# Performance work log

Hardware: AMD Instinct MI355X
Metric: run time of the kernel (lower is better)

## Reference

```python
import math
import jax, jax.numpy as jnp
from jax import lax
import numpy as np

SQRT2 = 1.4142135623730951
LR_MLP = 0.01


def _blur_kernel():
    k = jnp.array([1., 3., 3., 1.], dtype=jnp.float32)
    k = k[:, None] * k[None, :]
    return k / jnp.sum(k)


def upfirdn2d(x, kernel, up, pad0, pad1):
    # x: (B,C,H,W). Matches torch upfirdn2d_native (flip kernel, zero-upsample, pad, correlate).
    B, C, H, W = x.shape
    x = x.reshape(B * C, 1, H, W)
    k = jnp.flip(kernel, (0, 1))[None, None]
    p1 = pad1 + (up - 1)  # lax lhs_dilation omits trailing zeros of upfirdn upsampling
    out = lax.conv_general_dilated(x, k, (1, 1), ((pad0, p1), (pad0, p1)), lhs_dilation=(up, up))
    return out.reshape(B, C, out.shape[-2], out.shape[-1])


def pixel_norm(x, eps=1e-6):
    norm = jnp.sqrt(jnp.sum(x * x, axis=1, keepdims=True))
    norm = norm / math.sqrt(x.shape[1])
    return x / (norm + eps)


def fused_act(x, b):
    return jax.nn.leaky_relu(x + b[None, :, None, None], 0.2) * SQRT2


def mod_conv(x, w, sw, sb, lat, demodulate, up):
    # w: (Cout,Cin,kh,kw); sw: (Cin, style_ch) equalized-lr linear; lat: (B, style_ch)
    Cout, Cin, kh, kw = w.shape
    s = lat @ (sw.T * (1.0 / math.sqrt(sw.shape[1]))) + sb  # (B, Cin), bias_init=1
    wm = (w * (1.0 / math.sqrt(Cin * kh * kw)))[None] * s[:, None, :, None, None]
    if demodulate:
        d = lax.rsqrt(jnp.sum(wm * wm, axis=(2, 3, 4)) + 1e-8)
        wm = wm * d[:, :, None, None, None]
    if up:
        # per-sample conv_transpose(stride=2, pad=0) == dilated conv with flipped kernel
        def f(xi, wi):
            return lax.conv_general_dilated(xi[None], jnp.flip(wi, (2, 3)), (1, 1),
                                            ((kh - 1, kh - 1), (kw - 1, kw - 1)),
                                            lhs_dilation=(2, 2))[0]
        out = jax.vmap(f)(x, wm)
        out = upfirdn2d(out, _blur_kernel() * 4.0, 1, 1, 1)  # Blur pad=(1,1), k*factor^2
    else:
        pad = kh // 2
        def f(xi, wi):
            return lax.conv_general_dilated(xi[None], wi, (1, 1), ((pad, pad), (pad, pad)))[0]
        out = jax.vmap(f)(x, wm)
    return out


def style_mapping(z, W, Bv):
    x = pixel_norm(z)
    sc = 1.0 / math.sqrt(W.shape[-1])
    for i in range(W.shape[0]):
        x = jax.nn.leaky_relu(x @ (W[i].T * sc) + Bv[i] * LR_MLP, 0.2) * SQRT2
    return x


def setup_inputs() -> dict:
    key = jax.random.key(0)
    ks = jax.random.split(key, 32)
    B = 32
    inp = {
        'z': jax.random.normal(ks[0], (B, 512), jnp.float32),
        'mlp_w': jax.random.normal(ks[1], (8, 512, 512), jnp.float32),
        'mlp_b': jax.random.normal(ks[2], (8, 512), jnp.float32),
        'const_input': jax.random.normal(ks[3], (1, 512, 4, 4), jnp.float32),
        'conv_w': jax.random.normal(ks[4], (9, 512, 512, 3, 3), jnp.float32),
        'conv_style_w': jax.random.normal(ks[5], (9, 512, 512), jnp.float32),
        'conv_style_b': jnp.ones((9, 512), jnp.float32),
        'noise_w': jax.random.normal(ks[6], (9,), jnp.float32),
        'act_bias': jnp.zeros((9, 512), jnp.float32),
        'torgb_w': jax.random.normal(ks[7], (5, 3, 512, 1, 1), jnp.float32),
        'torgb_style_w': jax.random.normal(ks[8], (5, 512, 512), jnp.float32),
        'torgb_style_b': jnp.ones((5, 512), jnp.float32),
        'torgb_bias': jnp.zeros((5, 3), jnp.float32),
    }
    sizes = [4, 8, 8, 16, 16, 32, 32, 64, 64]
    for i, s in enumerate(sizes):
        inp[f'noise{i}'] = jax.random.normal(ks[10 + i], (B, 1, s, s), jnp.float32)
    return inp


def reference(z, mlp_w, mlp_b, const_input, conv_w, conv_style_w, conv_style_b,
              noise_w, act_bias, torgb_w, torgb_style_w, torgb_style_b, torgb_bias,
              noise0, noise1, noise2, noise3, noise4, noise5, noise6, noise7, noise8):
    noises = [noise0, noise1, noise2, noise3, noise4, noise5, noise6, noise7, noise8]
    w = style_mapping(z, mlp_w, mlp_b)  # single style injection -> same w for all layers
    B = z.shape[0]
    x = jnp.tile(const_input, (B, 1, 1, 1))

    def sconv(x, i, up):
        out = mod_conv(x, conv_w[i], conv_style_w[i], conv_style_b[i], w, True, up)
        out = out + noise_w[i] * noises[i]
        return fused_act(out, act_bias[i])

    def trgb(x, j):
        out = mod_conv(x, torgb_w[j], torgb_style_w[j], torgb_style_b[j], w, False, False)
        return out + torgb_bias[j][None, :, None, None]

    x = sconv(x, 0, False)
    skip = trgb(x, 0)
    bk = _blur_kernel() * 4.0
    for r in range(4):  # resolutions 8,16,32,64
        x = sconv(x, 1 + 2 * r, True)
        x = sconv(x, 2 + 2 * r, False)
        skip = trgb(x, r + 1) + upfirdn2d(skip, bk, 2, 2, 1)  # UpsampleUpFIRDn pad=(2,1)
    return skip  # (B,3,64,64)
```

## Files before the change

### kernel.cpp

```cpp
#include <hip/hip_runtime.h>
#include <hip/hip_bf16.h>
#include <cstdio>
#include <math.h>


static constexpr int NB = 32;
static constexpr float SQRT2F      = 1.41421356237309515f;
static constexpr float INV_SQRT512 = 0.04419417382415922f;
static constexpr float INV_SQRT4608= 0.014731391274719742f;

typedef __hip_bfloat16 bf16;
typedef __attribute__((ext_vector_type(8))) short bf16x8;
typedef __attribute__((ext_vector_type(4))) float f32x4;

__device__ __forceinline__ float lrelu_s2(float v){ return (v > 0.f ? v : 0.2f*v) * SQRT2F; }
__device__ __forceinline__ float bf_lo(unsigned u){ unsigned v = u << 16; return __builtin_bit_cast(float, v); }
__device__ __forceinline__ float bf_hi(unsigned u){ unsigned v = u & 0xffff0000u; return __builtin_bit_cast(float, v); }
__device__ __forceinline__ unsigned packbf2(float a, float b){
  bf16 ha = __float2bfloat16(a), hb = __float2bfloat16(b);
  unsigned short ra = __builtin_bit_cast(unsigned short, ha);
  unsigned short rb = __builtin_bit_cast(unsigned short, hb);
  return (unsigned)ra | ((unsigned)rb << 16);
}

__global__ void k_mapping(const float* __restrict__ z, const float* __restrict__ mlp_w,
                          const float* __restrict__ mlp_b, float* __restrict__ wlat){
  __shared__ float xb[512], yb[512], red[256];
  int b = blockIdx.x, t = threadIdx.x;
  float z0 = z[b*512 + t], z1 = z[b*512 + t + 256];
  red[t] = z0*z0 + z1*z1;
  __syncthreads();
  for(int s = 128; s > 0; s >>= 1){ if(t < s) red[t] += red[t+s]; __syncthreads(); }
  float norm = sqrtf(red[0]) * INV_SQRT512;
  float inv = 1.f / (norm + 1e-6f);
  xb[t] = z0*inv; xb[t+256] = z1*inv;
  __syncthreads();
  for(int l = 0; l < 8; l++){
    const float* Wl = mlp_w + (size_t)l*512*512;
    const float* bl = mlp_b + l*512;
    for(int oo = 0; oo < 2; oo++){
      int o = t + oo*256;
      const float4* wr = (const float4*)(Wl + (size_t)o*512);
      float acc = 0.f;
      #pragma unroll 4
      for(int k = 0; k < 128; k++){
        float4 w4 = wr[k];
        acc += w4.x*xb[4*k] + w4.y*xb[4*k+1] + w4.z*xb[4*k+2] + w4.w*xb[4*k+3];
      }
      yb[o] = lrelu_s2(acc*INV_SQRT512 + bl[o]*0.01f);
    }
    __syncthreads();
    xb[t] = yb[t]; xb[t+256] = yb[t+256];
    __syncthreads();
  }
  wlat[b*512+t] = xb[t]; wlat[b*512+t+256] = xb[t+256];
}

__global__ void k_styles(const float* __restrict__ wlat,
                         const float* __restrict__ csw, const float* __restrict__ csb,
                         const float* __restrict__ tsw, const float* __restrict__ tsb,
                         float* __restrict__ s_conv, float* __restrict__ s_trgb){
  int gid = blockIdx.x*256 + threadIdx.x;
  int l = gid >> 14;
  int b = (gid >> 9) & 31;
  int i = gid & 511;
  const float* row; float bias, wsc;
  if(l < 9){ row = csw + ((size_t)l*512 + i)*512; bias = csb[l*512+i]; wsc = INV_SQRT4608; }
  else     { int lt = l-9; row = tsw + ((size_t)lt*512 + i)*512; bias = tsb[lt*512+i]; wsc = INV_SQRT512; }
  const float4* r4 = (const float4*)row;
  const float4* w4 = (const float4*)(wlat + b*512);
  float acc = 0.f;
  #pragma unroll 4
  for(int k = 0; k < 128; k++){
    float4 a = w4[k], c = r4[k];
    acc += a.x*c.x + a.y*c.y + a.z*c.z + a.w*c.w;
  }
  float s = (acc*INV_SQRT512 + bias) * wsc;
  if(l < 9) s_conv[((size_t)l*32 + b)*512 + i] = s;
  else      s_trgb[((size_t)(l-9)*32 + b)*512 + i] = s;
}

__global__ void k_prep(const float* __restrict__ cw, float* __restrict__ wsq,
                       bf16* __restrict__ wB){
  int gid = blockIdx.x*256 + threadIdx.x;
  const float* p = cw + (size_t)gid*9;
  int l = gid >> 18;
  int oi = gid & 0x3ffff;
  float v[9]; float a = 0.f;
  #pragma unroll
  for(int t = 0; t < 9; t++){ v[t] = p[t]; a += v[t]*v[t]; }
  wsq[gid] = a;
  #pragma unroll
  for(int tap = 0; tap < 9; tap++)
    wB[((size_t)(l*9 + tap) << 18) + oi] = __float2bfloat16(v[tap]);
}

__global__ void k_demod(const float* __restrict__ s_conv, const float* __restrict__ wsq,
                        float* __restrict__ d_conv){
  __shared__ float s2[512];
  int l = blockIdx.x/32, b = blockIdx.x%32, t = threadIdx.x;
  size_t base = ((size_t)l*32 + b)*512;
  float v0 = s_conv[base + t], v1 = s_conv[base + t + 256];
  s2[t] = v0*v0; s2[t+256] = v1*v1;
  __syncthreads();
  for(int oo = 0; oo < 2; oo++){
    int o = t + oo*256;
    const float4* wr = (const float4*)(wsq + ((size_t)l*512 + o)*512);
    float acc = 0.f;
    #pragma unroll 4
    for(int k = 0; k < 128; k++){
      float4 w = wr[k];
      acc += w.x*s2[4*k] + w.y*s2[4*k+1] + w.z*s2[4*k+2] + w.w*s2[4*k+3];
    }
    d_conv[base + o] = rsqrtf(acc + 1e-8f);
  }
}

__global__ void k_ratio(const float* __restrict__ s_conv, const float* __restrict__ s_trgb,
                        float* __restrict__ rat){
  int gid = blockIdx.x*256 + threadIdx.x;
  int lt = gid >> 14;
  if(lt >= 4){ rat[gid] = 1.0f; return; }
  int b = (gid >> 9) & 31;
  int i = gid & 511;
  int cl = 1 + 2*lt;
  float st = s_trgb[((size_t)lt*32 + b)*512 + i];
  float sc = s_conv[((size_t)cl*32 + b)*512 + i];
  rat[gid] = (sc != 0.f) ? st/sc : 0.f;
}

__global__ void k_init(const float* __restrict__ ci, const float* __restrict__ s_conv,
                       bf16* __restrict__ act){
  int gid = blockIdx.x*256 + threadIdx.x;
  int c = gid & 511; int px = (gid >> 9) & 15; int b = gid >> 13;
  act[gid] = __float2bfloat16(ci[c*16 + px] * s_conv[b*512 + c]);
}

template<bool UP>
__global__ __launch_bounds__(256, 2)
void k_conv(const bf16* __restrict__ act, const bf16* __restrict__ wL,
            const float* __restrict__ dL, const float* __restrict__ noise,
            const float* __restrict__ nw_ptr, const float* __restrict__ ab,
            const float* __restrict__ sN, bf16* __restrict__ outp,
            int Hin, int Mblocks){
  const int q8 = gridDim.x >> 3;
  const int swz = (blockIdx.x & 7)*q8 + (blockIdx.x >> 3);
  const int nb = swz & 3, mb = swz >> 2;
  if(mb >= Mblocks) return;
  const int mbase = mb*128, nbase = nb*128;

  int py = 0, px = 0;
  int OHy, OHx;
  if(UP){
    int cls = blockIdx.z; py = cls >> 1; px = cls & 1;
    OHy = Hin + 1 - py; OHx = Hin + 1 - px;
  } else {
    OHy = Hin; OHx = Hin;
  }
  const int pixN = OHy*OHx;
  const int Mtot = NB*pixN;
  if(mbase >= Mtot) return;

  __shared__ short As[128*64];
  __shared__ short Bs[128*64];
  const int t = threadIdx.x;
  const int row  = t >> 1;
  const int half = t & 1;
  const int r7   = row & 7;

  int m = mbase + row;
  const bool mval = (m < Mtot);
  int mm = mval ? m : 0;
  const int gb = mm / pixN; int rem = mm % pixN;
  const int gY = rem / OHx, gX = rem % OHx;

  const int wid = t >> 6;
  const int mrow0 = (wid >> 1)*64;
  const int ncol0 = (wid & 1)*64;
  const int lr = t & 15;
  const int ks = (t & 63) >> 4;
  const int lr7 = lr & 7;
  const int sw0 = (ks ^ lr7)*8;
  const int sw1 = ((4 + ks) ^ lr7)*8;

  int wsl[4];
  #pragma unroll
  for(int j = 0; j < 4; j++) wsl[j] = ((half*4 + j) ^ r7)*8;

  f32x4 acc[4][4];
  #pragma unroll
  for(int i = 0; i < 4; i++)
    #pragma unroll
    for(int j = 0; j < 4; j++) acc[i][j] = (f32x4){0.f,0.f,0.f,0.f};

  int dyl[3], dxl[3], ndy, ndx;
  if(UP){
    if(py == 0){ dyl[0]=0; dyl[1]=2; ndy=2; } else { dyl[0]=1; ndy=1; }
    if(px == 0){ dxl[0]=0; dxl[1]=2; ndx=2; } else { dxl[0]=1; ndx=1; }
  } else {
    dyl[0]=0; dyl[1]=1; dyl[2]=2; ndy=3;
    dxl[0]=0; dxl[1]=1; dxl[2]=2; ndx=3;
  }
  const int TT = ndy*ndx;

  const bf16* browB = wL + ((size_t)(nbase + row) << 9) + half*32;

  for(int tt = 0; tt < TT; tt++){
    const int dy = dyl[tt/ndx], dx = dxl[tt%ndx];
    const int tap = dy*3 + dx;
    bool aok = false; const bf16* aptr = act;
    {
      int yy, xx;
      if(UP){ yy = gY - ((dy - py) >> 1); xx = gX - ((dx - px) >> 1); }
      else  { yy = gY + dy - 1;           xx = gX + dx - 1; }
      if(mval && (unsigned)yy < (unsigned)Hin && (unsigned)xx < (unsigned)Hin){
        aok = true;
        aptr = act + ((size_t)((gb*Hin + yy)*Hin + xx) << 9) + half*32;
      }
    }
    const bf16* bptr = browB + ((size_t)tap << 18);

    uint4 pa[4], pb[4];
    #pragma unroll
    for(int j = 0; j < 4; j++){
      pa[j] = aok ? *(const uint4*)(aptr + j*8) : make_uint4(0u,0u,0u,0u);
      pb[j] = *(const uint4*)(bptr + j*8);
    }

    #pragma unroll
    for(int c = 0; c < 8; c++){
      asm volatile("" ::: "memory");
      __builtin_amdgcn_s_barrier();
      #pragma unroll
      for(int j = 0; j < 4; j++){
        *(uint4*)&As[row*64 + wsl[j]] = pa[j];
        *(uint4*)&Bs[row*64 + wsl[j]] = pb[j];
      }
      uint4 na[4], nb4[4];
      if(c < 7){
        const int koff = (c+1)*64;
        #pragma unroll
        for(int j = 0; j < 4; j++){
          na[j]  = aok ? *(const uint4*)(aptr + koff + j*8) : make_uint4(0u,0u,0u,0u);
          nb4[j] = *(const uint4*)(bptr + koff + j*8);
        }
      }
      asm volatile("s_waitcnt lgkmcnt(0)" ::: "memory");
      __builtin_amdgcn_s_barrier();
      #pragma unroll
      for(int h = 0; h < 2; h++){
        const int swr = h ? sw1 : sw0;
        bf16x8 af[4], bfr[4];
        #pragma unroll
        for(int f = 0; f < 4; f++){
          af[f]  = *(const bf16x8*)&As[(mrow0 + f*16 + lr)*64 + swr];
          bfr[f] = *(const bf16x8*)&Bs[(ncol0 + f*16 + lr)*64 + swr];
        }
        #pragma unroll
        for(int mf = 0; mf < 4; mf++)
          #pragma unroll
          for(int nf = 0; nf < 4; nf++)
            acc[mf][nf] = __builtin_amdgcn_mfma_f32_16x16x32_bf16(af[mf], bfr[nf], acc[mf][nf], 0, 0, 0);
      }
      if(c < 7){
        #pragma unroll
        for(int j = 0; j < 4; j++){ pa[j] = na[j]; pb[j] = nb4[j]; }
      }
    }
  }

  const float nwv = UP ? 0.f : *nw_ptr;
  const int U = 2*Hin + 1;
  #pragma unroll
  for(int mf = 0; mf < 4; mf++){
    #pragma unroll
    for(int r = 0; r < 4; r++){
      int me = mbase + mrow0 + mf*16 + ks*4 + r;
      if(me >= Mtot) continue;
      int b = me / pixN; int rem2 = me % pixN; int y = rem2 / OHx, x = rem2 % OHx;
      const float* drow = dL + b*512;
      bf16* orow;
      float nz = 0.f; const float* srow = nullptr;
      if(UP){
        orow = outp + (((size_t)((b*U + 2*y + py))*U + (2*x + px)) << 9);
      } else {
        nz = nwv * noise[(b*OHy + y)*OHx + x];
        srow = sN + b*512;
        orow = outp + ((size_t)me << 9);
      }
      #pragma unroll
      for(int nf = 0; nf < 4; nf++){
        int n = nbase + ncol0 + nf*16 + lr;
        float val = acc[mf][nf][r] * drow[n];
        if(!UP) val = lrelu_s2(val + nz + ab[n]) * srow[n];
        orow[n] = __float2bfloat16(val);
      }
    }
  }
}

__global__ void k_blurV(const bf16* __restrict__ u, bf16* __restrict__ tmp, int O){
  const int U = O + 1;
  size_t gid = (size_t)blockIdx.x*256 + threadIdx.x;
  size_t total = (size_t)NB*O*U*128;
  if(gid >= total) return;
  int c4 = gid & 127;
  size_t pix = gid >> 7;
  int X = pix % U; int Y = (pix/U) % O; int b = pix/((size_t)O*U);
  const float k1[4] = {0.25f, 0.75f, 0.75f, 0.25f};
  float4 a = make_float4(0.f,0.f,0.f,0.f);
  #pragma unroll
  for(int ky = 0; ky < 4; ky++){
    int yy = Y + ky - 1; if(yy < 0 || yy >= U) continue;
    float w = k1[ky];
    uint2 u2 = *(const uint2*)(u + (((size_t)(b*U + yy)*U + X) << 9) + c4*4);
    a.x += w*bf_lo(u2.x); a.y += w*bf_hi(u2.x);
    a.z += w*bf_lo(u2.y); a.w += w*bf_hi(u2.y);
  }
  uint2 pk;
  pk.x = packbf2(a.x, a.y); pk.y = packbf2(a.z, a.w);
  *(uint2*)(tmp + (pix << 9) + c4*4) = pk;
}

__global__ void k_blurH(const bf16* __restrict__ tmp, const float* __restrict__ noise,
                        const float* __restrict__ nw_ptr, const float* __restrict__ ab,
                        const float* __restrict__ sN, bf16* __restrict__ act, int O){
  const int U = O + 1;
  size_t gid = (size_t)blockIdx.x*256 + threadIdx.x;
  size_t total = (size_t)NB*O*O*128;
  if(gid >= total) return;
  int c4 = gid & 127;
  size_t pix = gid >> 7;
  int X = pix % O; int Y = (pix/O) % O; int b = pix/((size_t)O*O);
  const float k1[4] = {0.25f, 0.75f, 0.75f, 0.25f};
  float4 a = make_float4(0.f,0.f,0.f,0.f);
  #pragma unroll
  for(int kx = 0; kx < 4; kx++){
    int xx = X + kx - 1; if(xx < 0 || xx >= U) continue;
    float w = k1[kx];
    uint2 u2 = *(const uint2*)(tmp + (((size_t)(b*O + Y)*U + xx) << 9) + c4*4);
    a.x += w*bf_lo(u2.x); a.y += w*bf_hi(u2.x);
    a.z += w*bf_lo(u2.y); a.w += w*bf_hi(u2.y);
  }
  float nz = (*nw_ptr) * noise[(b*O + Y)*O + X];
  const float* abp4 = ab + c4*4;
  float4 s4 = *(const float4*)(sN + b*512 + c4*4);
  uint2 pk;
  pk.x = packbf2(lrelu_s2(a.x + nz + abp4[0])*s4.x, lrelu_s2(a.y + nz + abp4[1])*s4.y);
  pk.y = packbf2(lrelu_s2(a.z + nz + abp4[2])*s4.z, lrelu_s2(a.w + nz + abp4[3])*s4.w);
  *(uint2*)(act + (pix << 9) + c4*4) = pk;
}

__global__ void k_torgb(const bf16* __restrict__ act, const float* __restrict__ tw,
                        const float* __restrict__ ratL, const float* __restrict__ tbias,
                        float* __restrict__ dst, int H, int lt, int addflag){
  int wid = threadIdx.x >> 6, lane = threadIdx.x & 63;
  int pix = blockIdx.x*4 + wid;
  int npix = NB*H*H;
  if(pix >= npix) return;
  int b = pix/(H*H);
  const bf16* ap = act + ((size_t)pix << 9);
  const float* rp = ratL + (size_t)b*512;
  const float* w0 = tw + ((size_t)lt*3 + 0)*512;
  const float* w1 = tw + ((size_t)lt*3 + 1)*512;
  const float* w2 = tw + ((size_t)lt*3 + 2)*512;
  float a0 = 0.f, a1 = 0.f, a2 = 0.f;
  #pragma unroll
  for(int j = 0; j < 8; j++){
    int i = lane + j*64;
    float xs = __bfloat162float(ap[i])*rp[i];
    a0 += xs*w0[i]; a1 += xs*w1[i]; a2 += xs*w2[i];
  }
  for(int off = 32; off > 0; off >>= 1){
    a0 += __shfl_xor(a0, off);
    a1 += __shfl_xor(a1, off);
    a2 += __shfl_xor(a2, off);
  }
  if(lane == 0){
    int rem = pix % (H*H);
    size_t o0 = ((size_t)(b*3 + 0)*H*H) + rem;
    size_t o1 = ((size_t)(b*3 + 1)*H*H) + rem;
    size_t o2 = ((size_t)(b*3 + 2)*H*H) + rem;
    float b0 = tbias[lt*3+0], b1 = tbias[lt*3+1], b2 = tbias[lt*3+2];
    if(addflag){ dst[o0] += a0 + b0; dst[o1] += a1 + b1; dst[o2] += a2 + b2; }
    else       { dst[o0]  = a0 + b0; dst[o1]  = a1 + b1; dst[o2]  = a2 + b2; }
  }
}

__global__ void k_skipup(const float* __restrict__ sin, float* __restrict__ sout, int h){
  const int O = 2*h;
  int gid = blockIdx.x*256 + threadIdx.x;
  int total = NB*3*O*O;
  if(gid >= total) return;
  int X = gid % O; int Y = (gid/O) % O; int c = (gid/(O*O)) % 3; int b = gid/(3*O*O);
  const float k1[4] = {1.f, 3.f, 3.f, 1.f};
  float acc = 0.f;
  for(int ky = (Y & 1); ky < 4; ky += 2){
    int ty = Y + ky - 2;
    if(ty < 0) continue;
    int y = ty >> 1; if(y >= h) continue;
    for(int kx = (X & 1); kx < 4; kx += 2){
      int tx = X + kx - 2;
      if(tx < 0) continue;
      int x = tx >> 1; if(x >= h) continue;
      acc += k1[ky]*k1[kx]*(1.f/16.f) * sin[((size_t)(b*3 + c)*h + y)*h + x];
    }
  }
  sout[gid] = acc;
}

extern "C" void kernel_launch(void* const* d_in, const int* in_sizes, int n_in,
                              void* d_out, int out_size, void* d_ws, size_t ws_size,
                              hipStream_t stream){
  const float* z     = (const float*)d_in[0];
  const float* mlp_w = (const float*)d_in[1];
  const float* mlp_b = (const float*)d_in[2];
  const float* cinp  = (const float*)d_in[3];
  const float* conv_w= (const float*)d_in[4];
  const float* csw   = (const float*)d_in[5];
  const float* csb   = (const float*)d_in[6];
  const float* nwp   = (const float*)d_in[7];
  const float* abp   = (const float*)d_in[8];
  const float* tw    = (const float*)d_in[9];
  const float* tsw   = (const float*)d_in[10];
  const float* tsb   = (const float*)d_in[11];
  const float* tb    = (const float*)d_in[12];
  const float* noise[9];
  for(int i = 0; i < 9; i++) noise[i] = (const float*)d_in[13 + i];

  const size_t UMAX = (size_t)32*65*65*512;
  char* base = (char*)d_ws;
  size_t off = 0;
  bf16* buf0 = (bf16*)(base + off); off += UMAX*2;
  bf16* buf1 = (bf16*)(base + off); off += UMAX*2;
  bf16* wB   = (bf16*)(base + off); off += (size_t)9*9*512*512*2;
  float* wsq = (float*)(base + off); off += (size_t)9*512*512*4;
  float* wlat= (float*)(base + off); off += (size_t)32*512*4;
  float* sconv=(float*)(base + off); off += (size_t)9*32*512*4;
  float* dconv=(float*)(base + off); off += (size_t)9*32*512*4;
  float* strgb=(float*)(base + off); off += (size_t)5*32*512*4;
  float* rat  =(float*)(base + off); off += (size_t)5*32*512*4;
  float* skipA=(float*)(base + off); off += (size_t)32*3*64*64*4;
  float* skipB=(float*)(base + off); off += (size_t)32*3*64*64*4;
  if(ws_size < off){
    fprintf(stderr, "kernel_launch: ws too small (%zu < %zu)\n", ws_size, off);
    return;
  }
  float* out = (float*)d_out;

  k_mapping<<<32, 256, 0, stream>>>(z, mlp_w, mlp_b, wlat);
  k_styles <<<896, 256, 0, stream>>>(wlat, csw, csb, tsw, tsb, sconv, strgb);
  k_prep   <<<9216, 256, 0, stream>>>(conv_w, wsq, wB);
  k_demod  <<<288, 256, 0, stream>>>(sconv, wsq, dconv);
  k_ratio  <<<320, 256, 0, stream>>>(sconv, strgb, rat);
  k_init   <<<1024, 256, 0, stream>>>(cinp, sconv, buf0);

  auto conv_noup = [&](const bf16* in, bf16* o, int H, int layer, const float* sN){
    int M = 32*H*H; int Mb = (M + 127)/128;
    int Gx = ((Mb*4 + 7)/8)*8;
    k_conv<false><<<dim3(Gx,1,1), 256, 0, stream>>>(in, wB + ((size_t)layer*9 << 18),
        dconv + (size_t)layer*NB*512, noise[layer], nwp + layer, abp + layer*512, sN, o, H, Mb);
  };
  auto conv_up = [&](const bf16* in, bf16* o, int Hin, int layer){
    int Mmax = 32*(Hin+1)*(Hin+1); int Mb = (Mmax + 127)/128;
    int Gx = ((Mb*4 + 7)/8)*8;
    k_conv<true><<<dim3(Gx,1,4), 256, 0, stream>>>(in, wB + ((size_t)layer*9 << 18),
        dconv + (size_t)layer*NB*512, nullptr, nullptr, nullptr, nullptr, o, Hin, Mb);
  };
  auto blur = [&](const bf16* u, bf16* tmp, bf16* o, int O, int layer, const float* sN){
    size_t totV = (size_t)32*O*(O+1)*128;
    size_t totH = (size_t)32*O*O*128;
    k_blurV<<<(unsigned)((totV + 255)/256), 256, 0, stream>>>(u, tmp, O);
    k_blurH<<<(unsigned)((totH + 255)/256), 256, 0, stream>>>(tmp, noise[layer], nwp + layer,
        abp + layer*512, sN, o, O);
  };
  auto torgb = [&](const bf16* act, float* dst, int H, int lt, int add){
    int npix = 32*H*H;
    k_torgb<<<(npix + 3)/4, 256, 0, stream>>>(act, tw, rat + (size_t)lt*NB*512, tb, dst, H, lt, add);
  };
  auto skipup = [&](const float* sin, float* sout, int h){
    int total = 32*3*(2*h)*(2*h);
    k_skipup<<<(total + 255)/256, 256, 0, stream>>>(sin, sout, h);
  };

  const float* S = sconv;
  const float* sT4 = strgb + (size_t)4*NB*512;

  conv_noup(buf0, buf1, 4, 0, S + (size_t)1*NB*512);
  torgb(buf1, skipA, 4, 0, 0);

  conv_up(buf1, buf0, 4, 1);
  blur(buf0, buf1, buf0, 8, 1, S + (size_t)2*NB*512);
  conv_noup(buf0, buf1, 8, 2, S + (size_t)3*NB*512);
  skipup(skipA, skipB, 4);
  torgb(buf1, skipB, 8, 1, 1);

  conv_up(buf1, buf0, 8, 3);
  blur(buf0, buf1, buf0, 16, 3, S + (size_t)4*NB*512);
  conv_noup(buf0, buf1, 16, 4, S + (size_t)5*NB*512);
  skipup(skipB, skipA, 8);
  torgb(buf1, skipA, 16, 2, 1);

  conv_up(buf1, buf0, 16, 5);
  blur(buf0, buf1, buf0, 32, 5, S + (size_t)6*NB*512);
  conv_noup(buf0, buf1, 32, 6, S + (size_t)7*NB*512);
  skipup(skipA, skipB, 16);
  torgb(buf1, skipB, 32, 3, 1);

  conv_up(buf1, buf0, 32, 7);
  blur(buf0, buf1, buf0, 64, 7, S + (size_t)8*NB*512);
  conv_noup(buf0, buf1, 64, 8, sT4);
  skipup(skipB, out, 32);
  torgb(buf1, out, 64, 4, 1);
}
```

Before: 2.204 ms.

## Add 256x256-tile implicit-GEMM conv kernel for large non-upsampling layers

Adds k_conv2, a 512-thread implicit-GEMM 3x3 conv kernel with 256x256 output tiles and register-prefetched global loads double-staged into swizzled LDS. It is used for non-upsampling layers at 32x32 and 64x64, and the original 128-tile kernel is kept for smaller resolutions. The larger tiles are meant to raise arithmetic intensity and cut repeated weight and activation loads. In exchange each thread holds 32 accumulator vectors (high register pressure at launch bounds 512,2), uses 64KB of shared memory per block, and launches fewer blocks.

```diff
diff --git a/kernel.cpp b/kernel.cpp
--- a/kernel.cpp
+++ b/kernel.cpp
@@ -299,6 +299,141 @@
   }
 }
 
+__global__ __launch_bounds__(512, 2)
+void k_conv2(const bf16* __restrict__ act, const bf16* __restrict__ wL,
+             const float* __restrict__ dL, const float* __restrict__ noise,
+             const float* __restrict__ nw_ptr, const float* __restrict__ ab,
+             const float* __restrict__ sN, bf16* __restrict__ outp,
+             int Hin, int Mblocks){
+  const int q8 = gridDim.x >> 3;
+  const int swz = (blockIdx.x & 7)*q8 + (blockIdx.x >> 3);
+  const int nb = swz & 1, mb = swz >> 1;
+  if(mb >= Mblocks) return;
+  const int mbase = mb*256, nbase = nb*256;
+  const int pixN = Hin*Hin;
+  const int Mtot = NB*pixN;
+  if(mbase >= Mtot) return;
+
+  __shared__ short As[256*64];
+  __shared__ short Bs[256*64];
+  const int t = threadIdx.x;
+  const int row  = t >> 1;
+  const int half = t & 1;
+  const int r7   = row & 7;
+
+  int m = mbase + row;
+  const bool mval = (m < Mtot);
+  int mm = mval ? m : 0;
+  const int gb = mm / pixN; int rem = mm % pixN;
+  const int gY = rem / Hin, gX = rem % Hin;
+
+  const int wid = t >> 6;
+  const int mrow0 = (wid >> 2)*128;
+  const int ncol0 = (wid & 3)*64;
+  const int lr = t & 15;
+  const int ks = (t & 63) >> 4;
+  const int lr7 = lr & 7;
+  const int sw0 = (ks ^ lr7)*8;
+  const int sw1 = ((4 + ks) ^ lr7)*8;
+
+  int wsl[4];
+  #pragma unroll
+  for(int j = 0; j < 4; j++) wsl[j] = ((half*4 + j) ^ r7)*8;
+
+  f32x4 acc[8][4];
+  #pragma unroll
+  for(int i = 0; i < 8; i++)
+    #pragma unroll
+    for(int j = 0; j < 4; j++) acc[i][j] = (f32x4){0.f,0.f,0.f,0.f};
+
+  const bf16* browB = wL + ((size_t)(nbase + row) << 9) + half*32;
+
+  for(int tt = 0; tt < 9; tt++){
+    const int dy = tt/3, dx = tt - dy*3;
+    const int tap = tt;
+    bool aok = false; const bf16* aptr = act;
+    {
+      int yy = gY + dy - 1, xx = gX + dx - 1;
+      if(mval && (unsigned)yy < (unsigned)Hin && (unsigned)xx < (unsigned)Hin){
+        aok = true;
+        aptr = act + ((size_t)((gb*Hin + yy)*Hin + xx) << 9) + half*32;
+      }
+    }
+    const bf16* bptr = browB + ((size_t)tap << 18);
+
+    uint4 pa[4], pb[4];
+    #pragma unroll
+    for(int j = 0; j < 4; j++){
+      pa[j] = aok ? *(const uint4*)(aptr + j*8) : make_uint4(0u,0u,0u,0u);
+      pb[j] = *(const uint4*)(bptr + j*8);
+    }
+
+    #pragma unroll
+    for(int c = 0; c < 8; c++){
+      asm volatile("" ::: "memory");
+      __builtin_amdgcn_s_barrier();
+      #pragma unroll
+      for(int j = 0; j < 4; j++){
+        *(uint4*)&As[row*64 + wsl[j]] = pa[j];
+        *(uint4*)&Bs[row*64 + wsl[j]] = pb[j];
+      }
+      uint4 na[4], nb4[4];
+      if(c < 7){
+        const int koff = (c+1)*64;
+        #pragma unroll
+        for(int j = 0; j < 4; j++){
+          na[j]  = aok ? *(const uint4*)(aptr + koff + j*8) : make_uint4(0u,0u,0u,0u);
+          nb4[j] = *(const uint4*)(bptr + koff + j*8);
+        }
+      }
+      asm volatile("s_waitcnt lgkmcnt(0)" ::: "memory");
+      __builtin_amdgcn_s_barrier();
+      #pragma unroll
+      for(int h = 0; h < 2; h++){
+        const int swr = h ? sw1 : sw0;
+        bf16x8 af[8], bfr[4];
+        #pragma unroll
+        for(int f = 0; f < 8; f++)
+          af[f]  = *(const bf16x8*)&As[(mrow0 + f*16 + lr)*64 + swr];
+        #pragma unroll
+        for(int f = 0; f < 4; f++)
+          bfr[f] = *(const bf16x8*)&Bs[(ncol0 + f*16 + lr)*64 + swr];
+        #pragma unroll
+        for(int mf = 0; mf < 8; mf++)
+          #pragma unroll
+          for(int nf = 0; nf < 4; nf++)
+            acc[mf][nf] = __builtin_amdgcn_mfma_f32_16x16x32_bf16(af[mf], bfr[nf], acc[mf][nf], 0, 0, 0);
+      }
+      if(c < 7){
+        #pragma unroll
+        for(int j = 0; j < 4; j++){ pa[j] = na[j]; pb[j] = nb4[j]; }
+      }
+    }
+  }
+
+  const float nwv = *nw_ptr;
+  #pragma unroll
+  for(int mf = 0; mf < 8; mf++){
+    #pragma unroll
+    for(int r = 0; r < 4; r++){
+      int me = mbase + mrow0 + mf*16 + ks*4 + r;
+      if(me >= Mtot) continue;
+      int b = me / pixN; int rem2 = me % pixN; int y = rem2 / Hin, x = rem2 % Hin;
+      const float* drow = dL + b*512;
+      float nz = nwv * noise[(b*Hin + y)*Hin + x];
+      const float* srow = sN + b*512;
+      bf16* orow = outp + ((size_t)me << 9);
+      #pragma unroll
+      for(int nf = 0; nf < 4; nf++){
+        int n = nbase + ncol0 + nf*16 + lr;
+        float val = acc[mf][nf][r] * drow[n];
+        val = lrelu_s2(val + nz + ab[n]) * srow[n];
+        orow[n] = __float2bfloat16(val);
+      }
+    }
+  }
+}
+
 __global__ void k_blurV(const bf16* __restrict__ u, bf16* __restrict__ tmp, int O){
   const int U = O + 1;
   size_t gid = (size_t)blockIdx.x*256 + threadIdx.x;
@@ -456,10 +591,17 @@
   k_init   <<<1024, 256, 0, stream>>>(cinp, sconv, buf0);
 
   auto conv_noup = [&](const bf16* in, bf16* o, int H, int layer, const float* sN){
-    int M = 32*H*H; int Mb = (M + 127)/128;
-    int Gx = ((Mb*4 + 7)/8)*8;
-    k_conv<false><<<dim3(Gx,1,1), 256, 0, stream>>>(in, wB + ((size_t)layer*9 << 18),
-        dconv + (size_t)layer*NB*512, noise[layer], nwp + layer, abp + layer*512, sN, o, H, Mb);
+    if(H >= 32){
+      int M = 32*H*H; int Mb = (M + 255)/256;
+      int Gx = ((Mb*2 + 7)/8)*8;
+      k_conv2<<<dim3(Gx,1,1), 512, 0, stream>>>(in, wB + ((size_t)layer*9 << 18),
+          dconv + (size_t)layer*NB*512, noise[layer], nwp + layer, abp + layer*512, sN, o, H, Mb);
+    } else {
+      int M = 32*H*H; int Mb = (M + 127)/128;
+      int Gx = ((Mb*4 + 7)/8)*8;
+      k_conv<false><<<dim3(Gx,1,1), 256, 0, stream>>>(in, wB + ((size_t)layer*9 << 18),
+          dconv + (size_t)layer*NB*512, noise[layer], nwp + layer, abp + layer*512, sN, o, H, Mb);
+    }
   };
   auto conv_up = [&](const bf16* in, bf16* o, int Hin, int layer){
     int Mmax = 32*(Hin+1)*(Hin+1); int Mb = (Mmax + 127)/128;
```

Measured after the change: 2.165 ms. Within noise of the previous version (-1.7%).

## Double-buffer conv GEMM tiles via direct global-to-LDS loads across taps

Applied to the files above, without the earlier changes.

Replaces the register-staged global→LDS copy in the implicit-GEMM conv with global_load_lds direct loads into double-buffered shared tiles. The next K-chunk, or the first chunk of the next tap, is prefetched while MFMAs run on the current buffer. Out-of-bounds rows point at a zeroed scratch page instead of using predicated zeros. This is meant to hide global load latency and cut VGPR pressure. It doubles LDS use to 64KB per block, which may limit occupancy with launch_bounds(256,2), and it depends on correct vmcnt accounting.

```diff
diff --git a/kernel.cpp b/kernel.cpp
--- a/kernel.cpp
+++ b/kernel.cpp
@@ -12,6 +12,10 @@
 typedef __hip_bfloat16 bf16;
 typedef __attribute__((ext_vector_type(8))) short bf16x8;
 typedef __attribute__((ext_vector_type(4))) float f32x4;
+
+#define GLOAD_LDS16(src, dst) __builtin_amdgcn_global_load_lds( \
+    (const __attribute__((address_space(1))) void*)(src), \
+    (__attribute__((address_space(3))) void*)(dst), 16, 0, 0)
 
 __device__ __forceinline__ float lrelu_s2(float v){ return (v > 0.f ? v : 0.2f*v) * SQRT2F; }
 __device__ __forceinline__ float bf_lo(unsigned u){ unsigned v = u << 16; return __builtin_bit_cast(float, v); }
@@ -142,10 +146,10 @@
             const float* __restrict__ dL, const float* __restrict__ noise,
             const float* __restrict__ nw_ptr, const float* __restrict__ ab,
             const float* __restrict__ sN, bf16* __restrict__ outp,
-            int Hin, int Mblocks){
+            const bf16* __restrict__ zp, int Hin, int Mblocks){
   const int q8 = gridDim.x >> 3;
-  const int swz = (blockIdx.x & 7)*q8 + (blockIdx.x >> 3);
-  const int nb = swz & 3, mb = swz >> 2;
+  const int swzb = (blockIdx.x & 7)*q8 + (blockIdx.x >> 3);
+  const int nb = swzb & 3, mb = swzb >> 2;
   if(mb >= Mblocks) return;
   const int mbase = mb*128, nbase = nb*128;
 
@@ -161,20 +165,25 @@
   const int Mtot = NB*pixN;
   if(mbase >= Mtot) return;
 
-  __shared__ short As[128*64];
-  __shared__ short Bs[128*64];
+  __shared__ short As[2][128*64];
+  __shared__ short Bs[2][128*64];
   const int t = threadIdx.x;
-  const int row  = t >> 1;
-  const int half = t & 1;
-  const int r7   = row & 7;
-
-  int m = mbase + row;
-  const bool mval = (m < Mtot);
-  int mm = mval ? m : 0;
-  const int gb = mm / pixN; int rem = mm % pixN;
-  const int gY = rem / OHx, gX = rem % OHx;
-
-  const int wid = t >> 6;
+  const int wid  = t >> 6;
+  const int lane = t & 63;
+  const int rloc = lane >> 3;
+  const int slot = lane & 7;
+
+  int swz[4]; int gbv[4], gYv[4], gXv[4]; bool mv[4];
+  const bf16* bB[4];
+  #pragma unroll
+  for(int i = 0; i < 4; i++){
+    int r = wid*32 + i*8 + rloc;
+    swz[i] = slot ^ (r & 7);
+    int m = mbase + r; mv[i] = (m < Mtot); int mm = mv[i] ? m : 0;
+    gbv[i] = mm / pixN; int rem = mm % pixN; gYv[i] = rem / OHx; gXv[i] = rem % OHx;
+    bB[i] = wL + ((size_t)(nbase + r) << 9) + swz[i]*8;
+  }
+
   const int mrow0 = (wid >> 1)*64;
   const int ncol0 = (wid & 1)*64;
   const int lr = t & 15;
@@ -183,10 +192,6 @@
   const int sw0 = (ks ^ lr7)*8;
   const int sw1 = ((4 + ks) ^ lr7)*8;
 
-  int wsl[4];
-  #pragma unroll
-  for(int j = 0; j < 4; j++) wsl[j] = ((half*4 + j) ^ r7)*8;
-
   f32x4 acc[4][4];
   #pragma unroll
   for(int i = 0; i < 4; i++)
@@ -203,49 +208,46 @@
   }
   const int TT = ndy*ndx;
 
-  const bf16* browB = wL + ((size_t)(nbase + row) << 9) + half*32;
+  auto mkA = [&](int dy, int dx, const bf16** aA){
+    #pragma unroll
+    for(int i = 0; i < 4; i++){
+      int yy, xx;
+      if(UP){ yy = gYv[i] - ((dy - py) >> 1); xx = gXv[i] - ((dx - px) >> 1); }
+      else  { yy = gYv[i] + dy - 1;           xx = gXv[i] + dx - 1; }
+      bool ok = mv[i] && ((unsigned)yy < (unsigned)Hin) && ((unsigned)xx < (unsigned)Hin);
+      aA[i] = ok ? (act + (((size_t)((gbv[i]*Hin + yy)*Hin + xx)) << 9) + swz[i]*8) : zp;
+    }
+  };
+  auto issue = [&](const bf16** aA, int tapIdx, int c, int bb){
+    #pragma unroll
+    for(int i = 0; i < 4; i++)
+      GLOAD_LDS16(aA[i] + c*64, &As[bb][(wid*32 + i*8)*64]);
+    #pragma unroll
+    for(int i = 0; i < 4; i++)
+      GLOAD_LDS16(bB[i] + ((size_t)tapIdx << 18) + c*64, &Bs[bb][(wid*32 + i*8)*64]);
+  };
+
+  const bf16* aC[4]; const bf16* aN[4];
+  int tapC = dyl[0]*3 + dxl[0], tapN = 0;
+  mkA(dyl[0], dxl[0], aC);
+  issue(aC, tapC, 0, 0);
 
   for(int tt = 0; tt < TT; tt++){
-    const int dy = dyl[tt/ndx], dx = dxl[tt%ndx];
-    const int tap = dy*3 + dx;
-    bool aok = false; const bf16* aptr = act;
-    {
-      int yy, xx;
-      if(UP){ yy = gY - ((dy - py) >> 1); xx = gX - ((dx - px) >> 1); }
-      else  { yy = gY + dy - 1;           xx = gX + dx - 1; }
-      if(mval && (unsigned)yy < (unsigned)Hin && (unsigned)xx < (unsigned)Hin){
-        aok = true;
-        aptr = act + ((size_t)((gb*Hin + yy)*Hin + xx) << 9) + half*32;
-      }
-    }
-    const bf16* bptr = browB + ((size_t)tap << 18);
-
-    uint4 pa[4], pb[4];
-    #pragma unroll
-    for(int j = 0; j < 4; j++){
-      pa[j] = aok ? *(const uint4*)(aptr + j*8) : make_uint4(0u,0u,0u,0u);
-      pb[j] = *(const uint4*)(bptr + j*8);
-    }
-
+    const bool haveNextTap = (tt + 1 < TT);
+    if(haveNextTap){
+      int dyN = dyl[(tt+1)/ndx], dxN = dxl[(tt+1)%ndx];
+      tapN = dyN*3 + dxN;
+      mkA(dyN, dxN, aN);
+    }
     #pragma unroll
     for(int c = 0; c < 8; c++){
-      asm volatile("" ::: "memory");
-      __builtin_amdgcn_s_barrier();
-      #pragma unroll
-      for(int j = 0; j < 4; j++){
-        *(uint4*)&As[row*64 + wsl[j]] = pa[j];
-        *(uint4*)&Bs[row*64 + wsl[j]] = pb[j];
-      }
-      uint4 na[4], nb4[4];
-      if(c < 7){
-        const int koff = (c+1)*64;
-        #pragma unroll
-        for(int j = 0; j < 4; j++){
-          na[j]  = aok ? *(const uint4*)(aptr + koff + j*8) : make_uint4(0u,0u,0u,0u);
-          nb4[j] = *(const uint4*)(bptr + koff + j*8);
-        }
-      }
-      asm volatile("s_waitcnt lgkmcnt(0)" ::: "memory");
+      const int bb = c & 1;
+      bool issued = true;
+      if(c < 7)               issue(aC, tapC, c+1, bb^1);
+      else if(haveNextTap)    issue(aN, tapN, 0,   bb^1);
+      else                    issued = false;
+      if(issued) asm volatile("s_waitcnt vmcnt(8)" ::: "memory");
+      else       asm volatile("s_waitcnt vmcnt(0)" ::: "memory");
       __builtin_amdgcn_s_barrier();
       #pragma unroll
       for(int h = 0; h < 2; h++){
@@ -253,8 +255,8 @@
         bf16x8 af[4], bfr[4];
         #pragma unroll
         for(int f = 0; f < 4; f++){
-          af[f]  = *(const bf16x8*)&As[(mrow0 + f*16 + lr)*64 + swr];
-          bfr[f] = *(const bf16x8*)&Bs[(ncol0 + f*16 + lr)*64 + swr];
+          af[f]  = *(const bf16x8*)&As[bb][(mrow0 + f*16 + lr)*64 + swr];
+          bfr[f] = *(const bf16x8*)&Bs[bb][(ncol0 + f*16 + lr)*64 + swr];
         }
         #pragma unroll
         for(int mf = 0; mf < 4; mf++)
@@ -262,10 +264,13 @@
           for(int nf = 0; nf < 4; nf++)
             acc[mf][nf] = __builtin_amdgcn_mfma_f32_16x16x32_bf16(af[mf], bfr[nf], acc[mf][nf], 0, 0, 0);
       }
-      if(c < 7){
-        #pragma unroll
-        for(int j = 0; j < 4; j++){ pa[j] = na[j]; pb[j] = nb4[j]; }
-      }
+      asm volatile("s_waitcnt lgkmcnt(0)" ::: "memory");
+      __builtin_amdgcn_s_barrier();
+    }
+    if(haveNextTap){
+      #pragma unroll
+      for(int i = 0; i < 4; i++) aC[i] = aN[i];
+      tapC = tapN;
     }
   }
 
@@ -442,12 +447,14 @@
   float* rat  =(float*)(base + off); off += (size_t)5*32*512*4;
   float* skipA=(float*)(base + off); off += (size_t)32*3*64*64*4;
   float* skipB=(float*)(base + off); off += (size_t)32*3*64*64*4;
+  bf16* zpage=(bf16*)(base + off); off += 2048;
   if(ws_size < off){
     fprintf(stderr, "kernel_launch: ws too small (%zu < %zu)\n", ws_size, off);
     return;
   }
   float* out = (float*)d_out;
 
+  hipMemsetAsync(zpage, 0, 2048, stream);
   k_mapping<<<32, 256, 0, stream>>>(z, mlp_w, mlp_b, wlat);
   k_styles <<<896, 256, 0, stream>>>(wlat, csw, csb, tsw, tsb, sconv, strgb);
   k_prep   <<<9216, 256, 0, stream>>>(conv_w, wsq, wB);
@@ -459,13 +466,13 @@
     int M = 32*H*H; int Mb = (M + 127)/128;
     int Gx = ((Mb*4 + 7)/8)*8;
     k_conv<false><<<dim3(Gx,1,1), 256, 0, stream>>>(in, wB + ((size_t)layer*9 << 18),
-        dconv + (size_t)layer*NB*512, noise[layer], nwp + layer, abp + layer*512, sN, o, H, Mb);
+        dconv + (size_t)layer*NB*512, noise[layer], nwp + layer, abp + layer*512, sN, o, zpage, H, Mb);
   };
   auto conv_up = [&](const bf16* in, bf16* o, int Hin, int layer){
     int Mmax = 32*(Hin+1)*(Hin+1); int Mb = (Mmax + 127)/128;
     int Gx = ((Mb*4 + 7)/8)*8;
     k_conv<true><<<dim3(Gx,1,4), 256, 0, stream>>>(in, wB + ((size_t)layer*9 << 18),
-        dconv + (size_t)layer*NB*512, nullptr, nullptr, nullptr, nullptr, o, Hin, Mb);
+        dconv + (size_t)layer*NB*512, nullptr, nullptr, nullptr, nullptr, o, zpage, Hin, Mb);
   };
   auto blur = [&](const bf16* u, bf16* tmp, bf16* o, int O, int layer, const float* sN){
     size_t totV = (size_t)32*O*(O+1)*128;
```

New measurement: 2.130 ms. -3.4%, faster.
